# Kernel tuning notes

Measured on AMD Instinct MI355X. Metric: run time of the kernel, lower is better.

## Reference

```python
import jax, jax.numpy as jnp
import numpy as np

B, T = 256, 40
IN, E, H, V = 2048, 512, 1024, 5000


def setup_inputs() -> dict:
    key = jax.random.key(0)
    ks = jax.random.split(key, 12)
    s = 0.02
    X = jax.random.normal(ks[0], (B, IN), dtype=jnp.float32)
    labels = jax.random.randint(ks[1], (B, T), 0, V, dtype=jnp.int64)
    W_f = jax.random.normal(ks[2], (E, IN), dtype=jnp.float32) * s
    b_f = jnp.zeros((E,), dtype=jnp.float32)
    emb = jax.random.normal(ks[3], (V + 1, E), dtype=jnp.float32) * s
    emb = emb.at[V].set(0.0)  # padding_idx = vocab_size
    W_ih = jax.random.normal(ks[4], (4 * H, 2 * E), dtype=jnp.float32) * s
    W_hh = jax.random.normal(ks[5], (4 * H, H), dtype=jnp.float32) * s
    b_ih = jnp.zeros((4 * H,), dtype=jnp.float32)
    b_hh = jnp.zeros((4 * H,), dtype=jnp.float32)
    W_out = jax.random.normal(ks[6], (V, H), dtype=jnp.float32) * s
    b_out = jnp.zeros((V,), dtype=jnp.float32)
    return {"X": X, "labels": labels, "W_f": W_f, "b_f": b_f, "emb": emb,
            "W_ih": W_ih, "W_hh": W_hh, "b_ih": b_ih, "b_hh": b_hh,
            "W_out": W_out, "b_out": b_out}


def reference(X, labels, W_f, b_f, emb, W_ih, W_hh, b_ih, b_hh, W_out, b_out):
    features = X @ W_f.T + b_f                      # [B, E]
    embs = emb[labels]                              # [B, T, E]
    # step 0 uses embeddings[:, -1]; step i>0 uses embeddings[:, i-1]
    shifted = jnp.concatenate([embs[:, -1:, :], embs[:, :-1, :]], axis=1)  # [B,T,E]
    # precompute input-side gate contributions for all timesteps
    # input at step i is cat(features, shifted[:, i]) -> [B, 2E]
    gates_feat = features @ W_ih[:, :E].T           # [B, 4H], constant per step
    gates_emb = jnp.einsum('bte,ge->btg', shifted, W_ih[:, E:])  # [B, T, 4H]
    gates_x = gates_emb + (gates_feat + b_ih + b_hh)[:, None, :]  # [B, T, 4H]
    gates_x = jnp.transpose(gates_x, (1, 0, 2))     # [T, B, 4H]

    def step(carry, gx):
        h, c = carry
        g = gx + h @ W_hh.T                         # [B, 4H]
        i, f, gg, o = jnp.split(g, 4, axis=-1)      # torch LSTMCell gate order
        c = jax.nn.sigmoid(f) * c + jax.nn.sigmoid(i) * jnp.tanh(gg)
        h = jax.nn.sigmoid(o) * jnp.tanh(c)
        return (h, c), h

    h0 = jnp.zeros((X.shape[0], W_hh.shape[1]), dtype=X.dtype)
    c0 = jnp.zeros_like(h0)
    _, hs = jax.lax.scan(step, (h0, c0), gates_x)   # hs: [T, B, H]
    logits = jnp.einsum('tbh,vh->btv', hs, W_out) + b_out  # [B, T, V]
    return logits
```

## Files before the change

kernel.cpp:

```cpp
#include <hip/hip_runtime.h>
#include <hip/hip_bf16.h>
#include <math.h>

#define B_  256
#define T_  40
#define IN_ 2048
#define E_  512
#define H_  1024
#define V_  5000
#define G4_ 4096

typedef __bf16 bf16x8 __attribute__((ext_vector_type(8)));
typedef float  f32x4  __attribute__((ext_vector_type(4)));
typedef unsigned int u32x4 __attribute__((ext_vector_type(4)));
typedef unsigned short u16x8 __attribute__((ext_vector_type(8)));

__device__ __forceinline__ float sigm_f(float x) { return 1.0f / (1.0f + __expf(-x)); }
__device__ __forceinline__ float tanh_f(float x) { return 1.0f - 2.0f / (1.0f + __expf(2.0f * x)); }

__device__ __forceinline__ unsigned short f2b(float x) {
    __hip_bfloat16 h = __float2bfloat16(x);
    return *reinterpret_cast<unsigned short*>(&h);
}
__device__ __forceinline__ float b2f(unsigned short u) {
    unsigned int v = (unsigned int)u << 16;
    return __builtin_bit_cast(float, v);
}

#define GLOAD_LDS(g, l) __builtin_amdgcn_global_load_lds(                     \
    (const __attribute__((address_space(1))) unsigned int*)(g),               \
    (__attribute__((address_space(3))) unsigned int*)(l), 16, 0, 0)

__device__ __forceinline__ void l2_load16(u32x4* dst, const unsigned short* p) {
    asm volatile("global_load_dwordx4 %0, %1, off" : "=v"(*dst) : "v"(p));
}
__device__ __forceinline__ void llc_store16(unsigned short* p, u32x4 v) {
    asm volatile("global_store_dwordx4 %0, %1, off sc0 sc1" :: "v"(p), "v"(v) : "memory");
}
__device__ __forceinline__ void llc_store4(unsigned int* p, unsigned int v) {
    asm volatile("global_store_dword %0, %1, off sc0 sc1" :: "v"(p), "v"(v) : "memory");
}
__device__ __forceinline__ unsigned int llc_load4_wait(const unsigned int* p) {
    unsigned int v;
    asm volatile("global_load_dword %0, %1, off sc0 sc1\n\ts_waitcnt vmcnt(0)"
                 : "=v"(v) : "v"(p) : "memory");
    return v;
}
#define VM_WAIT(n) do {                                                       \
    asm volatile("s_waitcnt vmcnt(" #n ")" ::: "memory");                     \
    __builtin_amdgcn_sched_barrier(0);                                        \
} while (0)

template<int OUTMODE>
__global__ __launch_bounds__(256) void gemm_mfma(
    const unsigned short* __restrict__ A, int lda, int aBlocked,
    const int* __restrict__ gidx,
    const unsigned short* __restrict__ Bm, int ldb, int bMapQ,
    const float* __restrict__ bias,
    const float* __restrict__ addMat, int rowMask, long long addStride,
    void* __restrict__ Cout, int ldc, int N, int K)
{
    __shared__ unsigned short SH[24576];

    const int tid  = threadIdx.x;
    const int wave = tid >> 6, lane = tid & 63;
    const int brow0 = blockIdx.y * 128, bcol0 = blockIdx.x * 128;
    const int wrow0 = (wave >> 1) * 64, wcol0 = (wave & 1) * 64;

    const int srow = lane >> 2;
    const int scol = (lane & 3) * 8;
    const size_t kstep = aBlocked ? 256 : 1;
    const unsigned short *pA[2], *pB[2];
    int segoff[2];
    #pragma unroll
    for (int i = 0; i < 2; ++i) {
        int seg = wave * 2 + i;
        int row = seg * 16 + srow;
        long long ar = gidx ? (long long)gidx[brow0 + row] : (long long)(brow0 + row);
        if (aBlocked)
            pA[i] = A + ((size_t)ar << 4) + ((size_t)(scol >> 4) << 12) + (scol & 8);
        else
            pA[i] = A + (size_t)ar * lda + scol;
        int bc = bcol0 + row;
        long long wrow = bMapQ ? (long long)(((bc & 3) << 10) | (bc >> 2)) : bc;
        pB[i] = Bm + wrow * ldb + scol;
        segoff[i] = seg * 512;
    }

    f32x4 acc[4][4] = {};
    const int foff = (lane & 15) * 32 + (lane >> 4) * 8;

    #define STAGE(buf, k0)                                                    \
        GLOAD_LDS(pA[0] + (size_t)(k0) * kstep, SH + (buf) * 4096 + segoff[0]); \
        GLOAD_LDS(pA[1] + (size_t)(k0) * kstep, SH + (buf) * 4096 + segoff[1]); \
        GLOAD_LDS(pB[0] + (k0), SH + 12288 + (buf) * 4096 + segoff[0]);       \
        GLOAD_LDS(pB[1] + (k0), SH + 12288 + (buf) * 4096 + segoff[1]);

    STAGE(0, 0)
    STAGE(1, 32)

    int cur = 0;
    for (int k0 = 0; k0 < K; k0 += 32) {
        if (k0 + 32 < K) { VM_WAIT(4); } else { VM_WAIT(0); }
        __builtin_amdgcn_s_barrier();

        if (k0 + 64 < K) {
            int nb = cur + 2; if (nb >= 3) nb -= 3;
            STAGE(nb, k0 + 64)
        }

        bf16x8 a[4], b[4];
        #pragma unroll
        for (int m = 0; m < 4; ++m)
            a[m] = *(const bf16x8*)&SH[cur * 4096 + (wrow0 + m * 16) * 32 + foff];
        #pragma unroll
        for (int n = 0; n < 4; ++n)
            b[n] = *(const bf16x8*)&SH[12288 + cur * 4096 + (wcol0 + n * 16) * 32 + foff];
        #pragma unroll
        for (int m = 0; m < 4; ++m)
            #pragma unroll
            for (int n = 0; n < 4; ++n)
                acc[m][n] = __builtin_amdgcn_mfma_f32_16x16x32_bf16(
                    a[m], b[n], acc[m][n], 0, 0, 0);

        ++cur; if (cur == 3) cur = 0;
    }
    #undef STAGE

    if (OUTMODE == 0) {
        #pragma unroll
        for (int m = 0; m < 4; ++m)
            #pragma unroll
            for (int j = 0; j < 4; ++j) {
                int row = brow0 + wrow0 + m * 16 + (lane >> 4) * 4 + j;
                const float* addRow = addMat
                    ? addMat + (long long)(row & rowMask) * addStride : nullptr;
                #pragma unroll
                for (int n = 0; n < 4; ++n) {
                    int col = bcol0 + wcol0 + n * 16 + (lane & 15);
                    if (col < N) {
                        float v = acc[m][n][j];
                        if (addRow) v += addRow[col];
                        if (bias)   v += bias[col];
                        ((float*)Cout)[(long long)row * ldc + col] = v;
                    }
                }
            }
    } else if (OUTMODE == 1) {
        __syncthreads();
        #pragma unroll
        for (int m = 0; m < 4; ++m)
            #pragma unroll
            for (int j = 0; j < 4; ++j) {
                int lr = wrow0 + m * 16 + (lane >> 4) * 4 + j;
                int row = brow0 + lr;
                const float* addRow = addMat + (long long)(row & rowMask) * addStride;
                #pragma unroll
                for (int n = 0; n < 4; ++n) {
                    int lc = wcol0 + n * 16 + (lane & 15);
                    SH[lr * 128 + lc] = f2b(acc[m][n][j] + addRow[bcol0 + lc]);
                }
            }
        __syncthreads();
        #pragma unroll
        for (int p = 0; p < 8; ++p) {
            int idx = p * 256 + tid;
            int lr = idx >> 4, lc8 = (idx & 15) * 8;
            *(u32x4*)((unsigned short*)Cout + (size_t)(brow0 + lr) * ldc +
                      bcol0 + lc8) = *(const u32x4*)&SH[lr * 128 + lc8];
        }
    } else {
        #pragma unroll
        for (int m = 0; m < 4; ++m)
            #pragma unroll
            for (int j = 0; j < 4; ++j) {
                int row = brow0 + wrow0 + m * 16 + (lane >> 4) * 4 + j;
                #pragma unroll
                for (int n = 0; n < 4; ++n) {
                    int col = bcol0 + wcol0 + n * 16 + (lane & 15);
                    if (col < N)
                        ((unsigned short*)Cout)[(long long)row * ldc + col] =
                            f2b(acc[m][n][j] + (bias ? bias[col] : 0.f));
                }
            }
    }
}

__global__ __launch_bounds__(256, 2) void gemm_big(
    const unsigned short* __restrict__ A,
    const int* __restrict__ gidx,
    const unsigned short* __restrict__ Bm,
    const float* __restrict__ bias,
    float* __restrict__ C)
{
    __shared__ unsigned short SA[3 * 8192];
    __shared__ unsigned short SB[3 * 4096];

    const int tid = threadIdx.x;
    const int wave = tid >> 6, lane = tid & 63;
    const int brow0 = blockIdx.y * 256, bcol0 = blockIdx.x * 128;
    const int wrow0 = (wave >> 1) * 128, wcol0 = (wave & 1) * 64;

    const int srow = lane >> 2;
    const int scol = (lane & 3) * 8;
    const unsigned short* pA[4];
    const unsigned short* pB[2];
    int aoff[4], boff[2];
    #pragma unroll
    for (int i = 0; i < 4; ++i) {
        int seg = wave * 4 + i;
        int row = seg * 16 + srow;
        long long ar = gidx[brow0 + row];
        pA[i] = A + ((size_t)ar << 4) + ((size_t)(scol >> 4) << 12) + (scol & 8);
        aoff[i] = seg * 512;
    }
    #pragma unroll
    for (int i = 0; i < 2; ++i) {
        int seg = wave * 2 + i;
        int row = seg * 16 + srow;
        pB[i] = Bm + (size_t)(bcol0 + row) * 1024 + scol;
        boff[i] = seg * 512;
    }

    f32x4 acc[8][4] = {};
    const int foff = (lane & 15) * 32 + (lane >> 4) * 8;

    #define BSTAGE(buf, k0)                                                   \
        GLOAD_LDS(pA[0] + (size_t)(k0) * 256, SA + (buf) * 8192 + aoff[0]);   \
        GLOAD_LDS(pA[1] + (size_t)(k0) * 256, SA + (buf) * 8192 + aoff[1]);   \
        GLOAD_LDS(pA[2] + (size_t)(k0) * 256, SA + (buf) * 8192 + aoff[2]);   \
        GLOAD_LDS(pA[3] + (size_t)(k0) * 256, SA + (buf) * 8192 + aoff[3]);   \
        GLOAD_LDS(pB[0] + (k0), SB + (buf) * 4096 + boff[0]);                 \
        GLOAD_LDS(pB[1] + (k0), SB + (buf) * 4096 + boff[1]);

    BSTAGE(0, 0)
    BSTAGE(1, 32)

    int cur = 0;
    for (int k0 = 0; k0 < 1024; k0 += 32) {
        if (k0 + 32 < 1024) { VM_WAIT(6); } else { VM_WAIT(0); }
        __builtin_amdgcn_s_barrier();

        if (k0 + 64 < 1024) {
            int nb = cur + 2; if (nb >= 3) nb -= 3;
            BSTAGE(nb, k0 + 64)
        }

        bf16x8 b[4];
        #pragma unroll
        for (int n = 0; n < 4; ++n)
            b[n] = *(const bf16x8*)&SB[cur * 4096 + (wcol0 + n * 16) * 32 + foff];
        #pragma unroll
        for (int m = 0; m < 8; ++m) {
            bf16x8 a = *(const bf16x8*)&SA[cur * 8192 + (wrow0 + m * 16) * 32 + foff];
            #pragma unroll
            for (int n = 0; n < 4; ++n)
                acc[m][n] = __builtin_amdgcn_mfma_f32_16x16x32_bf16(
                    a, b[n], acc[m][n], 0, 0, 0);
        }
        ++cur; if (cur == 3) cur = 0;
    }
    #undef BSTAGE

    #pragma unroll
    for (int m = 0; m < 8; ++m)
        #pragma unroll
        for (int j = 0; j < 4; ++j) {
            int row = brow0 + wrow0 + m * 16 + (lane >> 4) * 4 + j;
            float* orow = C + (size_t)row * 5000;
            #pragma unroll
            for (int n = 0; n < 4; ++n) {
                int col = bcol0 + wcol0 + n * 16 + (lane & 15);
                if (col < V_)
                    orow[col] = acc[m][n][j] + bias[col];
            }
        }
}

__global__ __launch_bounds__(256) void recur_persist(
    unsigned short* __restrict__ hs,
    const unsigned short* __restrict__ Whh,
    const unsigned short* __restrict__ gates,
    unsigned int* __restrict__ flags)
{
    extern __shared__ unsigned short lds[];
    __shared__ unsigned short hstage[64][24];

    const int tid = threadIdx.x;
    const int w = tid >> 6, lane = tid & 63;
    const int mb = blockIdx.x >> 6;
    const int hb = blockIdx.x & 63;
    const int r16 = lane & 15, g4 = lane >> 4;
    const int sw7 = r16 & 7;
    const size_t SLOT = 262144;

    const int arow = mb * 64 + w * 16 + r16;
    const size_t abase = ((size_t)arow << 4) + ((g4 >> 1) << 12) + ((g4 & 1) << 3);
    const int orow0 = mb * 64 + w * 16 + g4 * 4;
    const int hc    = hb * 16 + r16;
    const int lrow0 = w * 16 + g4 * 4;
    const size_t gq_base = ((size_t)orow0 << 12) + ((size_t)hc << 2);

    ushort4 gqc[4], gqn[4];
    #pragma unroll
    for (int j = 0; j < 4; ++j)
        gqc[j] = *(const ushort4*)(gates + gq_base + ((size_t)j << 12));

    {
        const int q = w;
        for (int r = 0; r < 16; ++r) {
            const int g = q * 16 + r;
            const unsigned short* rowsrc =
                Whh + ((size_t)q * 1024 + hb * 16 + r) * H_;
            #pragma unroll
            for (int half = 0; half < 2; ++half) {
                int gran = (half * 64 + lane) ^ (g & 7);
                GLOAD_LDS(rowsrc + gran * 8, &lds[g * 1024 + half * 512]);
            }
        }
    }
    asm volatile("s_waitcnt vmcnt(0)" ::: "memory");
    __syncthreads();

    int qbase[4];
    #pragma unroll
    for (int q = 0; q < 4; ++q) qbase[q] = (q * 16 + r16) << 11;

    float cc[4];

    #define STORE_H(T1, HV)                                                   \
    {                                                                         \
        _Pragma("unroll")                                                     \
        for (int j = 0; j < 4; ++j) hstage[lrow0 + j][r16] = HV[j];           \
        __syncthreads();                                                      \
        if (w == 0) {                                                         \
            unsigned short* dst0 = hs + (size_t)(T1) * SLOT +                 \
                (((size_t)hb * 256 + mb * 64) << 4);                          \
            _Pragma("unroll")                                                 \
            for (int s = 0; s < 2; ++s) {                                     \
                int idx = s * 64 + lane;                                      \
                u32x4 v = *(const u32x4*)&hstage[idx >> 1][(idx & 1) * 8];    \
                llc_store16(dst0 + (size_t)idx * 8, v);                       \
            }                                                                 \
            asm volatile("s_waitcnt vmcnt(0)" ::: "memory");                  \
            if (lane == 0)                                                    \
                llc_store4(flags + ((T1) << 8) + (mb << 6) + hb, 1u);         \
        }                                                                     \
    }

    {
        #pragma unroll
        for (int j = 0; j < 4; ++j)
            gqn[j] = *(const ushort4*)(gates + (1ull << 20) + gq_base +
                                       ((size_t)j << 12));
        unsigned short hv[4];
        #pragma unroll
        for (int j = 0; j < 4; ++j) {
            float gi = b2f(gqc[j].x), gg = b2f(gqc[j].z), go = b2f(gqc[j].w);
            float c2 = sigm_f(gi) * tanh_f(gg);
            cc[j] = c2;
            hv[j] = f2b(sigm_f(go) * tanh_f(c2));
        }
        STORE_H(1, hv)
        #pragma unroll
        for (int j = 0; j < 4; ++j) gqc[j] = gqn[j];
    }

    for (int t = 1; t < T_; ++t) {
        {
            const unsigned int* fp = flags + ((size_t)t << 8) + (mb << 6) + lane;
            for (;;) {
                unsigned int fv = llc_load4_wait(fp);
                if (__all(fv == 1u)) break;
                __builtin_amdgcn_s_sleep(1);
            }
        }
        __builtin_amdgcn_sched_barrier(0);

        const unsigned short* hp = hs + (size_t)t * SLOT + abase;

        u32x4 a0[8], a1[8];
        #pragma unroll
        for (int u = 0; u < 8; ++u) l2_load16(&a0[u], hp + (size_t)u * 8192);
        #pragma unroll
        for (int u = 0; u < 8; ++u) l2_load16(&a1[u], hp + (size_t)(8 + u) * 8192);

        f32x4 acc[4] = {};

#define DO_CHUNK(BUF, KSB)                                                    \
        _Pragma("unroll")                                                     \
        for (int u = 0; u < 8; ++u) {                                         \
            bf16x8 a8 = __builtin_bit_cast(bf16x8, BUF[u]);                   \
            _Pragma("unroll")                                                 \
            for (int q = 0; q < 4; ++q) {                                     \
                int off = qbase[q] + (((((KSB) + u) * 4 + g4) ^ sw7) << 4);   \
                bf16x8 b8 = *(const bf16x8*)((const char*)lds + off);         \
                acc[q] = __builtin_amdgcn_mfma_f32_16x16x32_bf16(             \
                    a8, b8, acc[q], 0, 0, 0);                                 \
            }                                                                 \
        }

        VM_WAIT(8);
        DO_CHUNK(a0, 0)
        #pragma unroll
        for (int u = 0; u < 8; ++u) l2_load16(&a0[u], hp + (size_t)(16 + u) * 8192);
        VM_WAIT(8);
        DO_CHUNK(a1, 8)
        #pragma unroll
        for (int u = 0; u < 8; ++u) l2_load16(&a1[u], hp + (size_t)(24 + u) * 8192);
        VM_WAIT(8);
        DO_CHUNK(a0, 16)
        VM_WAIT(0);
        DO_CHUNK(a1, 24)
#undef DO_CHUNK

        if (t + 1 < T_) {
            #pragma unroll
            for (int j = 0; j < 4; ++j)
                gqn[j] = *(const ushort4*)(gates +
                    ((size_t)(t + 1) << 20) + gq_base + ((size_t)j << 12));
        }

        unsigned short hv[4];
        #pragma unroll
        for (int j = 0; j < 4; ++j) {
            float gi = acc[0][j] + b2f(gqc[j].x);
            float gf = acc[1][j] + b2f(gqc[j].y);
            float gg = acc[2][j] + b2f(gqc[j].z);
            float go = acc[3][j] + b2f(gqc[j].w);
            float c2 = sigm_f(gf) * cc[j] + sigm_f(gi) * tanh_f(gg);
            cc[j] = c2;
            hv[j] = f2b(sigm_f(go) * tanh_f(c2));
        }
        STORE_H(t + 1, hv)
        #pragma unroll
        for (int j = 0; j < 4; ++j) gqc[j] = gqn[j];
    }
    #undef STORE_H
}

__global__ void fused_prep(
    const float* __restrict__ emb, const float* __restrict__ W_ih,
    const float* __restrict__ W_hh, const float* __restrict__ W_out,
    const float* __restrict__ X, const float* __restrict__ W_f,
    const int* __restrict__ labels,
    const float* __restrict__ b_ih, const float* __restrict__ b_hh,
    unsigned short* __restrict__ emb_bf, unsigned short* __restrict__ WihE_bf,
    unsigned short* __restrict__ WihA_bf, unsigned short* __restrict__ Whh_bf,
    unsigned short* __restrict__ Wout_bf,
    unsigned short* __restrict__ X_bf, unsigned short* __restrict__ Wf_bf,
    int* __restrict__ idxEmb, int* __restrict__ idxLog,
    float* __restrict__ bsum_perm)
{
    const int i = blockIdx.x * 256 + threadIdx.x;

    if (i < B_ * T_) {
        {
            int t = i >> 8, b = i & (B_ - 1);
            int tsrc = (t == 0) ? (T_ - 1) : (t - 1);
            idxEmb[i] = labels[b * T_ + tsrc];
        }
        {
            int b = i / T_, t = i % T_;
            idxLog[i] = (t + 1) * 16384 + b;
        }
    }
    if (i < G4_) {
        int w = ((i & 3) << 10) | (i >> 2);
        bsum_perm[i] = b_ih[w] + b_hh[w];
    }

    const float* src = nullptr;
    unsigned short* dst = nullptr;
    bool zero = false;
    if (i < 640128) {
        int r = i >> 7, c4 = i & 127;
        src = emb + (size_t)r * 512 + c4 * 4;
        dst = emb_bf + (size_t)r * 512 + c4 * 4;
    } else if (i < 1164416) {
        int j = i - 640128, r = j >> 7, c4 = j & 127;
        src = W_ih + (size_t)r * 1024 + 512 + c4 * 4;
        dst = WihE_bf + (size_t)r * 512 + c4 * 4;
    } else if (i < 1688704) {
        int j = i - 1164416, r = j >> 7, c4 = j & 127;
        src = W_ih + (size_t)r * 1024 + c4 * 4;
        dst = WihA_bf + (size_t)r * 512 + c4 * 4;
    } else if (i < 2737280) {
        int j = i - 1688704, r = j >> 8, c4 = j & 255;
        src = W_hh + (size_t)r * 1024 + c4 * 4;
        dst = Whh_bf + (size_t)r * 1024 + c4 * 4;
    } else if (i < 4048000) {
        int j = i - 2737280, r = j >> 8, c4 = j & 255;
        zero = (r >= V_);
        src = W_out + (size_t)r * 1024 + c4 * 4;
        dst = Wout_bf + (size_t)r * 1024 + c4 * 4;
    } else if (i < 4179072) {
        int j = i - 4048000, r = j >> 9, c4 = j & 511;
        src = X + (size_t)r * 2048 + c4 * 4;
        dst = X_bf + (size_t)r * 2048 + c4 * 4;
    } else if (i < 4441216) {
        int j = i - 4179072, r = j >> 9, c4 = j & 511;
        src = W_f + (size_t)r * 2048 + c4 * 4;
        dst = Wf_bf + (size_t)r * 2048 + c4 * 4;
    } else {
        return;
    }

    ushort4 o;
    if (!zero) {
        float4 v = *(const float4*)src;
        o.x = f2b(v.x); o.y = f2b(v.y); o.z = f2b(v.z); o.w = f2b(v.w);
    } else {
        o = make_ushort4(0, 0, 0, 0);
    }
    *(ushort4*)dst = o;
}

extern "C" void kernel_launch(void* const* d_in, const int* in_sizes, int n_in,
                              void* d_out, int out_size, void* d_ws, size_t ws_size,
                              hipStream_t stream)
{
    const float* X      = (const float*)d_in[0];
    const int*   labels = (const int*)  d_in[1];
    const float* W_f    = (const float*)d_in[2];
    const float* b_f    = (const float*)d_in[3];
    const float* emb    = (const float*)d_in[4];
    const float* W_ih   = (const float*)d_in[5];
    const float* W_hh   = (const float*)d_in[6];
    const float* b_ih   = (const float*)d_in[7];
    const float* b_hh   = (const float*)d_in[8];
    const float* W_out  = (const float*)d_in[9];
    const float* b_out  = (const float*)d_in[10];
    float* out = (float*)d_out;
    (void)in_sizes; (void)n_in; (void)out_size; (void)ws_size;

    char* ws = (char*)d_ws;
    size_t off = 0;
    auto alloc = [&](size_t bytes) {
        void* p = ws + off;
        off += (bytes + 255) & ~(size_t)255;
        return p;
    };
    unsigned short* emb_bf  = (unsigned short*)alloc((size_t)(V_ + 1) * E_ * 2);
    unsigned short* WihE_bf = (unsigned short*)alloc((size_t)G4_ * E_ * 2);
    unsigned short* WihA_bf = (unsigned short*)alloc((size_t)G4_ * E_ * 2);
    unsigned short* Whh_bf  = (unsigned short*)alloc((size_t)G4_ * H_ * 2);
    unsigned short* Wout_bf = (unsigned short*)alloc((size_t)5120 * H_ * 2);
    unsigned short* hs_bf   = (unsigned short*)alloc((size_t)(T_ + 1) * 262144 * 2);
    unsigned short* feat_bf = (unsigned short*)alloc((size_t)B_ * E_ * 2);
    float* bsum_perm = (float*)alloc(G4_ * 4);
    int*   idxEmb    = (int*)  alloc(B_ * T_ * 4);
    int*   idxLog    = (int*)  alloc(B_ * T_ * 4);
    unsigned int* flags = (unsigned int*)alloc((size_t)(T_ + 1) * 256 * 4);

    unsigned short* gates_bf = (unsigned short*)out;
    float* baseMat = out + 22 * 1024 * 1024;
    unsigned short* X_bf  = (unsigned short*)(out + 25 * 1024 * 1024);
    unsigned short* Wf_bf = (unsigned short*)(out + 26 * 1024 * 1024);

    hipMemsetAsync(flags, 0, (size_t)(T_ + 1) * 256 * 4, stream);

    fused_prep<<<(4441216 + 255) / 256, 256, 0, stream>>>(
        emb, W_ih, W_hh, W_out, X, W_f, labels, b_ih, b_hh,
        emb_bf, WihE_bf, WihA_bf, Whh_bf, Wout_bf, X_bf, Wf_bf,
        idxEmb, idxLog, bsum_perm);

    gemm_mfma<2><<<dim3(E_ / 128, B_ / 128), 256, 0, stream>>>(
        X_bf, IN_, 0, nullptr, Wf_bf, IN_, 0, b_f,
        nullptr, 0, 0, feat_bf, E_, E_, IN_);

    gemm_mfma<0><<<dim3(G4_ / 128, B_ / 128), 256, 0, stream>>>(
        feat_bf, E_, 0, nullptr, WihA_bf, E_, 1, nullptr,
        bsum_perm, 0, 0, baseMat, G4_, G4_, E_);

    gemm_mfma<1><<<dim3(G4_ / 128, (B_ * T_) / 128), 256, 0, stream>>>(
        emb_bf, E_, 0, idxEmb, WihE_bf, E_, 1, nullptr,
        baseMat, B_ - 1, G4_, gates_bf, G4_, G4_, E_);

    {
        hipFuncSetAttribute((const void*)recur_persist,
                            hipFuncAttributeMaxDynamicSharedMemorySize, 131072);
        recur_persist<<<256, 256, 131072, stream>>>(hs_bf, Whh_bf, gates_bf, flags);
    }

    gemm_big<<<dim3(5120 / 128, 10240 / 256), 256, 0, stream>>>(
        hs_bf, idxLog, Wout_bf, b_out, out);
}
```

Measured before the change: 646.6 us.

## Poll per-k-group flags before each h chunk load and prefetch gates two steps ahead

New measurement: 637.9 us (median of 2 runs). No clear change (-1.3%).

```diff
diff --git a/kernel.cpp b/kernel.cpp
--- a/kernel.cpp
+++ b/kernel.cpp
@@ -301,10 +301,12 @@
     const int lrow0 = w * 16 + g4 * 4;
     const size_t gq_base = ((size_t)orow0 << 12) + ((size_t)hc << 2);
 
-    ushort4 gqc[4], gqn[4];
+    ushort4 gq0[4], gq1[4], gq2[4];
     #pragma unroll
-    for (int j = 0; j < 4; ++j)
-        gqc[j] = *(const ushort4*)(gates + gq_base + ((size_t)j << 12));
+    for (int j = 0; j < 4; ++j) {
+        gq0[j] = *(const ushort4*)(gates + gq_base + ((size_t)j << 12));
+        gq1[j] = *(const ushort4*)(gates + (1ull << 20) + gq_base + ((size_t)j << 12));
+    }
 
     {
         const int q = w;
@@ -348,44 +350,39 @@
         }                                                                     \
     }
 
+    #define POLL_GROUP(T, G)                                                  \
+    {                                                                         \
+        const unsigned int* fp = flags + ((size_t)(T) << 8) + (mb << 6) +     \
+                                 (G) * 16 + (lane & 15);                      \
+        for (;;) {                                                            \
+            unsigned int fv = llc_load4_wait(fp);                             \
+            if (__all(fv == 1u)) break;                                       \
+            __builtin_amdgcn_s_sleep(1);                                      \
+        }                                                                     \
+        __builtin_amdgcn_sched_barrier(0);                                    \
+    }
+
     {
-        #pragma unroll
-        for (int j = 0; j < 4; ++j)
-            gqn[j] = *(const ushort4*)(gates + (1ull << 20) + gq_base +
-                                       ((size_t)j << 12));
         unsigned short hv[4];
         #pragma unroll
         for (int j = 0; j < 4; ++j) {
-            float gi = b2f(gqc[j].x), gg = b2f(gqc[j].z), go = b2f(gqc[j].w);
+            float gi = b2f(gq0[j].x), gg = b2f(gq0[j].z), go = b2f(gq0[j].w);
             float c2 = sigm_f(gi) * tanh_f(gg);
             cc[j] = c2;
             hv[j] = f2b(sigm_f(go) * tanh_f(c2));
         }
         STORE_H(1, hv)
         #pragma unroll
-        for (int j = 0; j < 4; ++j) gqc[j] = gqn[j];
+        for (int j = 0; j < 4; ++j)
+            gq2[j] = *(const ushort4*)(gates + (2ull << 20) + gq_base +
+                                       ((size_t)j << 12));
+        #pragma unroll
+        for (int j = 0; j < 4; ++j) { gq0[j] = gq1[j]; gq1[j] = gq2[j]; }
     }
 
     for (int t = 1; t < T_; ++t) {
-        {
-            const unsigned int* fp = flags + ((size_t)t << 8) + (mb << 6) + lane;
-            for (;;) {
-                unsigned int fv = llc_load4_wait(fp);
-                if (__all(fv == 1u)) break;
-                __builtin_amdgcn_s_sleep(1);
-            }
-        }
-        __builtin_amdgcn_sched_barrier(0);
-
         const unsigned short* hp = hs + (size_t)t * SLOT + abase;
-
         u32x4 a0[8], a1[8];
-        #pragma unroll
-        for (int u = 0; u < 8; ++u) l2_load16(&a0[u], hp + (size_t)u * 8192);
-        #pragma unroll
-        for (int u = 0; u < 8; ++u) l2_load16(&a1[u], hp + (size_t)(8 + u) * 8192);
-
-        f32x4 acc[4] = {};
 
 #define DO_CHUNK(BUF, KSB)                                                    \
         _Pragma("unroll")                                                     \
@@ -400,43 +397,51 @@
             }                                                                 \
         }
 
-        VM_WAIT(8);
+        POLL_GROUP(t, 0)
+        #pragma unroll
+        for (int u = 0; u < 8; ++u) l2_load16(&a0[u], hp + (size_t)u * 8192);
+        POLL_GROUP(t, 1)
+        #pragma unroll
+        for (int u = 0; u < 8; ++u) l2_load16(&a1[u], hp + (size_t)(8 + u) * 8192);
+
+        f32x4 acc[4] = {};
         DO_CHUNK(a0, 0)
+        POLL_GROUP(t, 2)
         #pragma unroll
         for (int u = 0; u < 8; ++u) l2_load16(&a0[u], hp + (size_t)(16 + u) * 8192);
-        VM_WAIT(8);
         DO_CHUNK(a1, 8)
+        POLL_GROUP(t, 3)
         #pragma unroll
         for (int u = 0; u < 8; ++u) l2_load16(&a1[u], hp + (size_t)(24 + u) * 8192);
-        VM_WAIT(8);
         DO_CHUNK(a0, 16)
         VM_WAIT(0);
         DO_CHUNK(a1, 24)
 #undef DO_CHUNK
 
-        if (t + 1 < T_) {
-            #pragma unroll
-            for (int j = 0; j < 4; ++j)
-                gqn[j] = *(const ushort4*)(gates +
-                    ((size_t)(t + 1) << 20) + gq_base + ((size_t)j << 12));
-        }
-
         unsigned short hv[4];
         #pragma unroll
         for (int j = 0; j < 4; ++j) {
-            float gi = acc[0][j] + b2f(gqc[j].x);
-            float gf = acc[1][j] + b2f(gqc[j].y);
-            float gg = acc[2][j] + b2f(gqc[j].z);
-            float go = acc[3][j] + b2f(gqc[j].w);
+            float gi = acc[0][j] + b2f(gq0[j].x);
+            float gf = acc[1][j] + b2f(gq0[j].y);
+            float gg = acc[2][j] + b2f(gq0[j].z);
+            float go = acc[3][j] + b2f(gq0[j].w);
             float c2 = sigm_f(gf) * cc[j] + sigm_f(gi) * tanh_f(gg);
             cc[j] = c2;
             hv[j] = f2b(sigm_f(go) * tanh_f(c2));
         }
         STORE_H(t + 1, hv)
-        #pragma unroll
-        for (int j = 0; j < 4; ++j) gqc[j] = gqn[j];
+
+        if (t + 2 < T_) {
+            #pragma unroll
+            for (int j = 0; j < 4; ++j)
+                gq2[j] = *(const ushort4*)(gates +
+                    ((size_t)(t + 2) << 20) + gq_base + ((size_t)j << 12));
+        }
+        #pragma unroll
+        for (int j = 0; j < 4; ++j) { gq0[j] = gq1[j]; gq1[j] = gq2[j]; }
     }
     #undef STORE_H
+    #undef POLL_GROUP
 }
 
 __global__ void fused_prep(
```
